# Optimization experiments

Hardware: AMD Instinct MI355X
Metric: run time of the kernel (lower is better)

## Reference

```python
import jax, jax.numpy as jnp
import numpy as np

IN_F, OUT_F, TASK_D, RANK, HID = 1024, 1024, 256, 8, 64
ALPHA = 8.0
SCALING = ALPHA / RANK  # 1.0


def setup_inputs() -> dict:
    key = jax.random.key(0)
    ks = jax.random.split(key, 12)
    s = 0.02
    return {
        "x": jax.random.normal(ks[0], (4, 2048, IN_F), dtype=jnp.float32),
        "base_out": jax.random.normal(ks[1], (4, 2048, OUT_F), dtype=jnp.float32),
        "task_emb": jax.random.normal(ks[2], (4, TASK_D), dtype=jnp.float32),
        # gen_a MLP: Linear(task_dim->hid) + GELU + Linear(hid->out*r)
        "Wa1": jax.random.normal(ks[3], (HID, TASK_D), dtype=jnp.float32) * s,
        "ba1": jnp.zeros((HID,), dtype=jnp.float32),
        "Wa2": jax.random.normal(ks[4], (OUT_F * RANK, HID), dtype=jnp.float32) * s,
        "ba2": jnp.zeros((OUT_F * RANK,), dtype=jnp.float32),
        # gen_b MLP: Linear(task_dim->hid) + GELU + Linear(hid->r*in)
        "Wb1": jax.random.normal(ks[5], (HID, TASK_D), dtype=jnp.float32) * s,
        "bb1": jnp.zeros((HID,), dtype=jnp.float32),
        "Wb2": jax.random.normal(ks[6], (RANK * IN_F, HID), dtype=jnp.float32) * s,
        "bb2": jnp.zeros((RANK * IN_F,), dtype=jnp.float32),
    }


def reference(x, base_out, task_emb, Wa1, ba1, Wa2, ba2, Wb1, bb1, Wb2, bb2):
    lead = x.shape[:-1]
    x2d = x.reshape(-1, IN_F)                      # (b_eff, in)
    b_eff = x2d.shape[0]
    # broadcast task_emb to b_eff rows (repeat + trim, as in torch)
    B = task_emb.shape[0]
    reps = (b_eff + B - 1) // B
    task_eff = jnp.tile(task_emb, (reps, 1))[:b_eff]  # (b_eff, task_dim)

    gelu = lambda t: jax.nn.gelu(t, approximate=False)
    h_a = gelu(task_eff @ Wa1.T + ba1)
    vec_a = h_a @ Wa2.T + ba2                      # (b_eff, out*r)
    h_b = gelu(task_eff @ Wb1.T + bb1)
    vec_b = h_b @ Wb2.T + bb2                      # (b_eff, r*in)

    a = vec_a.reshape(b_eff, OUT_F, RANK)
    b = vec_b.reshape(b_eff, RANK, IN_F)

    # dropout p=0 (eval): x passes through
    tmp = jnp.einsum('bi,bri->br', x2d, b)         # (b_eff, r)
    y_delta = jnp.einsum('br,bor->bo', tmp, a)     # (b_eff, out)
    y = base_out.reshape(-1, OUT_F) + SCALING * y_delta
    return y.reshape(*lead, OUT_F)
```

## Files before the change

kernel.cpp:

```cpp
#include <hip/hip_runtime.h>
#include <math.h>

#define IN_F   1024
#define OUT_F  1024
#define TASK_D 256
#define RANK   8
#define HID    64

__device__ __forceinline__ float gelu_exact(float v) {
    return 0.5f * v * (1.0f + erff(v * 0.70710678118654752f));
}

__global__ __launch_bounds__(256) void gen_kernel(
    const float* __restrict__ task_emb,
    const float* __restrict__ Wa1, const float* __restrict__ ba1,
    const float* __restrict__ Wa2, const float* __restrict__ ba2,
    const float* __restrict__ Wb1, const float* __restrict__ bb1,
    const float* __restrict__ Wb2, const float* __restrict__ bb2,
    float* __restrict__ vec_a_t, float* __restrict__ vec_b)
{
    const int gen = blockIdx.x >> 7;
    const int blk = blockIdx.x & 127;
    const float* __restrict__ W1 = gen ? Wb1 : Wa1;
    const float* __restrict__ b1 = gen ? bb1 : ba1;
    const float* __restrict__ W2 = gen ? Wb2 : Wa2;
    const float* __restrict__ b2 = gen ? bb2 : ba2;

    __shared__ float hs[4][HID];
    {
        const int j = threadIdx.x >> 2;
        const int t = threadIdx.x & 3;
        const float4* te = (const float4*)(task_emb + t * TASK_D);
        const float4* w  = (const float4*)(W1 + j * TASK_D);
        float acc = 0.f;
        #pragma unroll
        for (int d = 0; d < TASK_D / 4; ++d) {
            float4 a = te[d], b = w[d];
            acc += a.x * b.x + a.y * b.y + a.z * b.z + a.w * b.w;
        }
        hs[t][j] = gelu_exact(acc + b1[j]);
    }
    __syncthreads();

    const int lrow = threadIdx.x >> 2;
    const int q    = threadIdx.x & 3;
    const int o    = blk * 64 + lrow;

    const float4* w2 = (const float4*)(W2 + (size_t)o * HID + q * 16);
    float acc0 = 0.f, acc1 = 0.f, acc2 = 0.f, acc3 = 0.f;
    #pragma unroll
    for (int k = 0; k < 4; ++k) {
        float4 w = w2[k];
        const int kb = q * 16 + k * 4;
        acc0 += hs[0][kb] * w.x + hs[0][kb+1] * w.y + hs[0][kb+2] * w.z + hs[0][kb+3] * w.w;
        acc1 += hs[1][kb] * w.x + hs[1][kb+1] * w.y + hs[1][kb+2] * w.z + hs[1][kb+3] * w.w;
        acc2 += hs[2][kb] * w.x + hs[2][kb+1] * w.y + hs[2][kb+2] * w.z + hs[2][kb+3] * w.w;
        acc3 += hs[3][kb] * w.x + hs[3][kb+1] * w.y + hs[3][kb+2] * w.z + hs[3][kb+3] * w.w;
    }
    #pragma unroll
    for (int off = 1; off <= 2; off <<= 1) {
        acc0 += __shfl_xor(acc0, off, 64);
        acc1 += __shfl_xor(acc1, off, 64);
        acc2 += __shfl_xor(acc2, off, 64);
        acc3 += __shfl_xor(acc3, off, 64);
    }
    if (q == 0) {
        const float bb = b2[o];
        float v[4] = { acc0 + bb, acc1 + bb, acc2 + bb, acc3 + bb };
        if (gen == 0) {
            const int oo = o >> 3, r = o & 7;
            #pragma unroll
            for (int t = 0; t < 4; ++t)
                vec_a_t[t * (RANK * OUT_F) + r * OUT_F + oo] = v[t];
        } else {
            #pragma unroll
            for (int t = 0; t < 4; ++t)
                vec_b[t * (RANK * IN_F) + o] = v[t];
        }
    }
}

__global__ __launch_bounds__(256, 8) void apply_kernel(
    const float* __restrict__ x, const float* __restrict__ base_out,
    const float* __restrict__ vec_a_t, const float* __restrict__ vec_b,
    float* __restrict__ out, int g_per_task)
{
    const int t    = blockIdx.x / g_per_task;
    const int g    = blockIdx.x % g_per_task;
    const int wave = threadIdx.x >> 6;
    const int ln   = threadIdx.x & 63;

    const int j   = g * 4 + wave;
    const int row = t + 4 * j;

    const float* __restrict__ xr = x + (size_t)row * IN_F;
    const float* __restrict__ bt = vec_b + (size_t)t * (RANK * IN_F);

    float4 xv[4];
    #pragma unroll
    for (int c = 0; c < 4; ++c)
        xv[c] = *(const float4*)(xr + c * 256 + ln * 4);

    float acc[RANK];
    #pragma unroll
    for (int r = 0; r < RANK; ++r) acc[r] = 0.f;

    #pragma unroll
    for (int c = 0; c < 4; ++c) {
        const int k = c * 256 + ln * 4;
        #pragma unroll
        for (int r = 0; r < RANK; ++r) {
            const float4 bv = *(const float4*)(bt + r * IN_F + k);
            acc[r] += xv[c].x * bv.x + xv[c].y * bv.y + xv[c].z * bv.z + xv[c].w * bv.w;
        }
    }

    #pragma unroll
    for (int off = 1; off <= 32; off <<= 1) {
        #pragma unroll
        for (int r = 0; r < RANK; ++r)
            acc[r] += __shfl_xor(acc[r], off, 64);
    }

    const float* __restrict__ at = vec_a_t + (size_t)t * (RANK * OUT_F);
    const float* __restrict__ br = base_out + (size_t)row * OUT_F;
    float* __restrict__ orow = out + (size_t)row * OUT_F;

    float4 bo[4];
    #pragma unroll
    for (int c = 0; c < 4; ++c)
        bo[c] = *(const float4*)(br + c * 256 + ln * 4);

    #pragma unroll
    for (int c = 0; c < 4; ++c) {
        const int o = c * 256 + ln * 4;
        float4 rv = bo[c];
        #pragma unroll
        for (int r = 0; r < RANK; ++r) {
            const float4 af = *(const float4*)(at + r * OUT_F + o);
            rv.x += acc[r] * af.x;
            rv.y += acc[r] * af.y;
            rv.z += acc[r] * af.z;
            rv.w += acc[r] * af.w;
        }
        *(float4*)(orow + o) = rv;
    }
}

extern "C" void kernel_launch(void* const* d_in, const int* in_sizes, int n_in,
                              void* d_out, int out_size, void* d_ws, size_t ws_size,
                              hipStream_t stream) {
    const float* x        = (const float*)d_in[0];
    const float* base_out = (const float*)d_in[1];
    const float* task_emb = (const float*)d_in[2];
    const float* Wa1      = (const float*)d_in[3];
    const float* ba1      = (const float*)d_in[4];
    const float* Wa2      = (const float*)d_in[5];
    const float* ba2      = (const float*)d_in[6];
    const float* Wb1      = (const float*)d_in[7];
    const float* bb1      = (const float*)d_in[8];
    const float* Wb2      = (const float*)d_in[9];
    const float* bb2      = (const float*)d_in[10];
    float* out = (float*)d_out;

    float* vec_a_t = (float*)d_ws;
    float* vec_b   = vec_a_t + 4 * RANK * OUT_F;

    const int b_eff = in_sizes[0] / IN_F;

    gen_kernel<<<256, 256, 0, stream>>>(task_emb, Wa1, ba1, Wa2, ba2,
                                        Wb1, bb1, Wb2, bb2, vec_a_t, vec_b);

    const int nblk = b_eff / 4;
    apply_kernel<<<nblk, 256, 0, stream>>>(x, base_out, vec_a_t, vec_b, out,
                                           nblk / 4);
}
```

Before: 156.6 us.

## Process four rows per wave with per-task B and A factors held in registers

Each wave now handles four rows of the same task instead of one. It loads the task's vec_b slice (8x1024) into registers once, reuses it for all four rows' rank projections, then reloads registers with the vec_a slice and reuses that for all four output rows. The aim is to cut repeated L2/global reads of the generated LoRA factors by four. The cost is a large register footprint (128 floats per lane for the tile), occupancy lowered to 2 blocks per CU, and a grid four times smaller.

Result: faster. 143.6 us (-8.3%).

```diff
diff --git a/kernel.cpp b/kernel.cpp
--- a/kernel.cpp
+++ b/kernel.cpp
@@ -80,70 +80,100 @@
     }
 }
 
-__global__ __launch_bounds__(256, 8) void apply_kernel(
+__global__ __launch_bounds__(256, 2) void apply_kernel(
     const float* __restrict__ x, const float* __restrict__ base_out,
     const float* __restrict__ vec_a_t, const float* __restrict__ vec_b,
-    float* __restrict__ out, int g_per_task)
+    float* __restrict__ out, int waves_per_task)
 {
-    const int t    = blockIdx.x / g_per_task;
-    const int g    = blockIdx.x % g_per_task;
     const int wave = threadIdx.x >> 6;
     const int ln   = threadIdx.x & 63;
-
-    const int j   = g * 4 + wave;
-    const int row = t + 4 * j;
-
-    const float* __restrict__ xr = x + (size_t)row * IN_F;
+    const int gw   = blockIdx.x * 4 + wave;
+    const int t    = gw / waves_per_task;
+    const int u    = gw % waves_per_task;
+
     const float* __restrict__ bt = vec_b + (size_t)t * (RANK * IN_F);
-
-    float4 xv[4];
-    #pragma unroll
-    for (int c = 0; c < 4; ++c)
-        xv[c] = *(const float4*)(xr + c * 256 + ln * 4);
-
-    float acc[RANK];
-    #pragma unroll
-    for (int r = 0; r < RANK; ++r) acc[r] = 0.f;
-
-    #pragma unroll
-    for (int c = 0; c < 4; ++c) {
-        const int k = c * 256 + ln * 4;
-        #pragma unroll
-        for (int r = 0; r < RANK; ++r) {
-            const float4 bv = *(const float4*)(bt + r * IN_F + k);
-            acc[r] += xv[c].x * bv.x + xv[c].y * bv.y + xv[c].z * bv.z + xv[c].w * bv.w;
-        }
-    }
-
-    #pragma unroll
-    for (int off = 1; off <= 32; off <<= 1) {
-        #pragma unroll
-        for (int r = 0; r < RANK; ++r)
-            acc[r] += __shfl_xor(acc[r], off, 64);
+    float4 tb[RANK][4];
+    #pragma unroll
+    for (int r = 0; r < RANK; ++r)
+        #pragma unroll
+        for (int c = 0; c < 4; ++c)
+            tb[r][c] = *(const float4*)(bt + r * IN_F + c * 256 + ln * 4);
+
+    float tmp[4][RANK];
+
+    #pragma unroll
+    for (int ii = 0; ii < 2; ++ii) {
+        float4 xv[2][4];
+        #pragma unroll
+        for (int i = 0; i < 2; ++i) {
+            const int row = t + 4 * (u * 4 + ii * 2 + i);
+            const float* __restrict__ xr = x + (size_t)row * IN_F;
+            #pragma unroll
+            for (int c = 0; c < 4; ++c)
+                xv[i][c] = *(const float4*)(xr + c * 256 + ln * 4);
+        }
+        #pragma unroll
+        for (int i = 0; i < 2; ++i) {
+            float acc[RANK];
+            #pragma unroll
+            for (int r = 0; r < RANK; ++r) acc[r] = 0.f;
+            #pragma unroll
+            for (int c = 0; c < 4; ++c) {
+                #pragma unroll
+                for (int r = 0; r < RANK; ++r) {
+                    const float4 bv = tb[r][c];
+                    acc[r] += xv[i][c].x * bv.x + xv[i][c].y * bv.y
+                            + xv[i][c].z * bv.z + xv[i][c].w * bv.w;
+                }
+            }
+            #pragma unroll
+            for (int off = 1; off <= 32; off <<= 1) {
+                #pragma unroll
+                for (int r = 0; r < RANK; ++r)
+                    acc[r] += __shfl_xor(acc[r], off, 64);
+            }
+            #pragma unroll
+            for (int r = 0; r < RANK; ++r) tmp[ii * 2 + i][r] = acc[r];
+        }
     }
 
     const float* __restrict__ at = vec_a_t + (size_t)t * (RANK * OUT_F);
-    const float* __restrict__ br = base_out + (size_t)row * OUT_F;
-    float* __restrict__ orow = out + (size_t)row * OUT_F;
-
-    float4 bo[4];
-    #pragma unroll
-    for (int c = 0; c < 4; ++c)
-        bo[c] = *(const float4*)(br + c * 256 + ln * 4);
-
-    #pragma unroll
-    for (int c = 0; c < 4; ++c) {
-        const int o = c * 256 + ln * 4;
-        float4 rv = bo[c];
-        #pragma unroll
-        for (int r = 0; r < RANK; ++r) {
-            const float4 af = *(const float4*)(at + r * OUT_F + o);
-            rv.x += acc[r] * af.x;
-            rv.y += acc[r] * af.y;
-            rv.z += acc[r] * af.z;
-            rv.w += acc[r] * af.w;
-        }
-        *(float4*)(orow + o) = rv;
+    #pragma unroll
+    for (int r = 0; r < RANK; ++r)
+        #pragma unroll
+        for (int c = 0; c < 4; ++c)
+            tb[r][c] = *(const float4*)(at + r * OUT_F + c * 256 + ln * 4);
+
+    #pragma unroll
+    for (int ii = 0; ii < 2; ++ii) {
+        float4 bo[2][4];
+        #pragma unroll
+        for (int i = 0; i < 2; ++i) {
+            const int row = t + 4 * (u * 4 + ii * 2 + i);
+            const float* __restrict__ br = base_out + (size_t)row * OUT_F;
+            #pragma unroll
+            for (int c = 0; c < 4; ++c)
+                bo[i][c] = *(const float4*)(br + c * 256 + ln * 4);
+        }
+        #pragma unroll
+        for (int i = 0; i < 2; ++i) {
+            const int row = t + 4 * (u * 4 + ii * 2 + i);
+            float* __restrict__ orow = out + (size_t)row * OUT_F;
+            #pragma unroll
+            for (int c = 0; c < 4; ++c) {
+                float4 rv = bo[i][c];
+                #pragma unroll
+                for (int r = 0; r < RANK; ++r) {
+                    const float4 af = tb[r][c];
+                    const float s = tmp[ii * 2 + i][r];
+                    rv.x += s * af.x;
+                    rv.y += s * af.y;
+                    rv.z += s * af.z;
+                    rv.w += s * af.w;
+                }
+                *(float4*)(orow + c * 256 + ln * 4) = rv;
+            }
+        }
     }
 }
 
@@ -171,7 +201,7 @@
     gen_kernel<<<256, 256, 0, stream>>>(task_emb, Wa1, ba1, Wa2, ba2,
                                         Wb1, bb1, Wb2, bb2, vec_a_t, vec_b);
 
-    const int nblk = b_eff / 4;
+    const int nblk = b_eff / 16;
     apply_kernel<<<nblk, 256, 0, stream>>>(x, base_out, vec_a_t, vec_b, out,
-                                           nblk / 4);
-}
+                                           nblk);
+}
```

## Split apply kernel into separate x·B projection and output update kernels

Applied to the files above, without the earlier changes.

Splits the fused apply kernel into two kernels. tmp_kernel computes the rank-8 projection of each x row and writes it to a workspace buffer. out_kernel loads the vec_a tile once per thread into registers and reuses it across four rows to add the low-rank update to base_out. The aim is to cut repeated reloads of vec_a and raise memory-level parallelism. The cost is an extra launch and a small intermediate write and read.

New measurement: 149.5 us. 1.05x faster.

```diff
diff --git a/kernel.cpp b/kernel.cpp
--- a/kernel.cpp
+++ b/kernel.cpp
@@ -80,18 +80,16 @@
     }
 }
 
-__global__ __launch_bounds__(256, 8) void apply_kernel(
-    const float* __restrict__ x, const float* __restrict__ base_out,
-    const float* __restrict__ vec_a_t, const float* __restrict__ vec_b,
-    float* __restrict__ out, int g_per_task)
+__global__ __launch_bounds__(256) void tmp_kernel(
+    const float* __restrict__ x, const float* __restrict__ vec_b,
+    float* __restrict__ tmp, int waves_per_task)
 {
-    const int t    = blockIdx.x / g_per_task;
-    const int g    = blockIdx.x % g_per_task;
     const int wave = threadIdx.x >> 6;
     const int ln   = threadIdx.x & 63;
-
-    const int j   = g * 4 + wave;
-    const int row = t + 4 * j;
+    const int gw   = blockIdx.x * 4 + wave;
+    const int t    = gw / waves_per_task;
+    const int j    = gw % waves_per_task;
+    const int row  = t + 4 * j;
 
     const float* __restrict__ xr = x + (size_t)row * IN_F;
     const float* __restrict__ bt = vec_b + (size_t)t * (RANK * IN_F);
@@ -122,28 +120,52 @@
             acc[r] += __shfl_xor(acc[r], off, 64);
     }
 
+    if (ln == 0) {
+        float* __restrict__ tr = tmp + (size_t)row * RANK;
+        *(float4*)(tr)     = make_float4(acc[0], acc[1], acc[2], acc[3]);
+        *(float4*)(tr + 4) = make_float4(acc[4], acc[5], acc[6], acc[7]);
+    }
+}
+
+__global__ __launch_bounds__(256, 4) void out_kernel(
+    const float* __restrict__ base_out, const float* __restrict__ vec_a_t,
+    const float* __restrict__ tmp, float* __restrict__ out,
+    int blocks_per_task)
+{
+    const int t = blockIdx.x / blocks_per_task;
+    const int g = blockIdx.x % blocks_per_task;
+    const int o = threadIdx.x * 4;
+
     const float* __restrict__ at = vec_a_t + (size_t)t * (RANK * OUT_F);
-    const float* __restrict__ br = base_out + (size_t)row * OUT_F;
-    float* __restrict__ orow = out + (size_t)row * OUT_F;
-
-    float4 bo[4];
-    #pragma unroll
-    for (int c = 0; c < 4; ++c)
-        bo[c] = *(const float4*)(br + c * 256 + ln * 4);
-
-    #pragma unroll
-    for (int c = 0; c < 4; ++c) {
-        const int o = c * 256 + ln * 4;
-        float4 rv = bo[c];
+    float4 af[RANK];
+    #pragma unroll
+    for (int r = 0; r < RANK; ++r)
+        af[r] = *(const float4*)(at + r * OUT_F + o);
+
+    int   row[4];
+    float4 bo[4], t0[4], t1[4];
+    #pragma unroll
+    for (int i = 0; i < 4; ++i) {
+        row[i] = t + 4 * (g * 4 + i);
+        bo[i] = *(const float4*)(base_out + (size_t)row[i] * OUT_F + o);
+        const float* __restrict__ tr = tmp + (size_t)row[i] * RANK;
+        t0[i] = *(const float4*)(tr);
+        t1[i] = *(const float4*)(tr + 4);
+    }
+
+    #pragma unroll
+    for (int i = 0; i < 4; ++i) {
+        const float s[RANK] = { t0[i].x, t0[i].y, t0[i].z, t0[i].w,
+                                t1[i].x, t1[i].y, t1[i].z, t1[i].w };
+        float4 rv = bo[i];
         #pragma unroll
         for (int r = 0; r < RANK; ++r) {
-            const float4 af = *(const float4*)(at + r * OUT_F + o);
-            rv.x += acc[r] * af.x;
-            rv.y += acc[r] * af.y;
-            rv.z += acc[r] * af.z;
-            rv.w += acc[r] * af.w;
-        }
-        *(float4*)(orow + o) = rv;
+            rv.x += s[r] * af[r].x;
+            rv.y += s[r] * af[r].y;
+            rv.z += s[r] * af[r].z;
+            rv.w += s[r] * af[r].w;
+        }
+        *(float4*)(out + (size_t)row[i] * OUT_F + o) = rv;
     }
 }
 
@@ -165,13 +187,17 @@
 
     float* vec_a_t = (float*)d_ws;
     float* vec_b   = vec_a_t + 4 * RANK * OUT_F;
+    float* tmp     = vec_b   + 4 * RANK * IN_F;
 
     const int b_eff = in_sizes[0] / IN_F;
 
     gen_kernel<<<256, 256, 0, stream>>>(task_emb, Wa1, ba1, Wa2, ba2,
                                         Wb1, bb1, Wb2, bb2, vec_a_t, vec_b);
 
-    const int nblk = b_eff / 4;
-    apply_kernel<<<nblk, 256, 0, stream>>>(x, base_out, vec_a_t, vec_b, out,
-                                           nblk / 4);
-}
+    const int nblk2 = b_eff / 4;
+    tmp_kernel<<<nblk2, 256, 0, stream>>>(x, vec_b, tmp, b_eff / 4);
+
+    const int nblk3 = b_eff / 4;
+    out_kernel<<<nblk3, 256, 0, stream>>>(base_out, vec_a_t, tmp, out,
+                                          nblk3 / 4);
+}
```

## Share LoRA A factors across rows via LDS and widen generator grid

Applied to the files above, without the earlier changes.

In the apply kernel, each wave still computes the rank-8 projection for its own row, but the results now go through shared memory. The output phase then has each thread load its slice of the A factors once and reuse it across the block's four rows, instead of reloading A per row. The generator kernel now uses 512 blocks of 32 output rows each, with an 8-lane reduction, to spread the weight-matrix reads over more blocks. This adds a block-wide barrier and lowers the occupancy hint from 8 to 6 blocks per CU.

New measurement: 151.3 us. 1.03x faster.

```diff
diff --git a/kernel.cpp b/kernel.cpp
--- a/kernel.cpp
+++ b/kernel.cpp
@@ -19,8 +19,8 @@
     const float* __restrict__ Wb2, const float* __restrict__ bb2,
     float* __restrict__ vec_a_t, float* __restrict__ vec_b)
 {
-    const int gen = blockIdx.x >> 7;
-    const int blk = blockIdx.x & 127;
+    const int gen = blockIdx.x >> 8;
+    const int blk = blockIdx.x & 255;
     const float* __restrict__ W1 = gen ? Wb1 : Wa1;
     const float* __restrict__ b1 = gen ? bb1 : ba1;
     const float* __restrict__ W2 = gen ? Wb2 : Wa2;
@@ -42,23 +42,23 @@
     }
     __syncthreads();
 
-    const int lrow = threadIdx.x >> 2;
-    const int q    = threadIdx.x & 3;
-    const int o    = blk * 64 + lrow;
+    const int lrow = threadIdx.x >> 3;
+    const int q    = threadIdx.x & 7;
+    const int o    = blk * 32 + lrow;
 
-    const float4* w2 = (const float4*)(W2 + (size_t)o * HID + q * 16);
+    const float4* w2 = (const float4*)(W2 + (size_t)o * HID + q * 8);
     float acc0 = 0.f, acc1 = 0.f, acc2 = 0.f, acc3 = 0.f;
     #pragma unroll
-    for (int k = 0; k < 4; ++k) {
+    for (int k = 0; k < 2; ++k) {
         float4 w = w2[k];
-        const int kb = q * 16 + k * 4;
+        const int kb = q * 8 + k * 4;
         acc0 += hs[0][kb] * w.x + hs[0][kb+1] * w.y + hs[0][kb+2] * w.z + hs[0][kb+3] * w.w;
         acc1 += hs[1][kb] * w.x + hs[1][kb+1] * w.y + hs[1][kb+2] * w.z + hs[1][kb+3] * w.w;
         acc2 += hs[2][kb] * w.x + hs[2][kb+1] * w.y + hs[2][kb+2] * w.z + hs[2][kb+3] * w.w;
         acc3 += hs[3][kb] * w.x + hs[3][kb+1] * w.y + hs[3][kb+2] * w.z + hs[3][kb+3] * w.w;
     }
     #pragma unroll
-    for (int off = 1; off <= 2; off <<= 1) {
+    for (int off = 1; off <= 4; off <<= 1) {
         acc0 += __shfl_xor(acc0, off, 64);
         acc1 += __shfl_xor(acc1, off, 64);
         acc2 += __shfl_xor(acc2, off, 64);
@@ -80,70 +80,86 @@
     }
 }
 
-__global__ __launch_bounds__(256, 8) void apply_kernel(
+__global__ __launch_bounds__(256, 6) void apply_kernel(
     const float* __restrict__ x, const float* __restrict__ base_out,
     const float* __restrict__ vec_a_t, const float* __restrict__ vec_b,
-    float* __restrict__ out, int g_per_task)
+    float* __restrict__ out, int blocks_per_task)
 {
-    const int t    = blockIdx.x / g_per_task;
-    const int g    = blockIdx.x % g_per_task;
+    const int t    = blockIdx.x / blocks_per_task;
+    const int g    = blockIdx.x % blocks_per_task;
     const int wave = threadIdx.x >> 6;
     const int ln   = threadIdx.x & 63;
 
-    const int j   = g * 4 + wave;
-    const int row = t + 4 * j;
+    __shared__ float tmps[4][RANK];
 
-    const float* __restrict__ xr = x + (size_t)row * IN_F;
-    const float* __restrict__ bt = vec_b + (size_t)t * (RANK * IN_F);
+    {
+        const int row = t + 4 * (g * 4 + wave);
+        const float* __restrict__ xr = x + (size_t)row * IN_F;
+        const float* __restrict__ bt = vec_b + (size_t)t * (RANK * IN_F);
 
-    float4 xv[4];
+        float4 xv[4];
+        #pragma unroll
+        for (int c = 0; c < 4; ++c)
+            xv[c] = *(const float4*)(xr + c * 256 + ln * 4);
+
+        float acc[RANK];
+        #pragma unroll
+        for (int r = 0; r < RANK; ++r) acc[r] = 0.f;
+
+        #pragma unroll
+        for (int c = 0; c < 4; ++c) {
+            const int k = c * 256 + ln * 4;
+            #pragma unroll
+            for (int r = 0; r < RANK; ++r) {
+                const float4 bv = *(const float4*)(bt + r * IN_F + k);
+                acc[r] += xv[c].x * bv.x + xv[c].y * bv.y
+                        + xv[c].z * bv.z + xv[c].w * bv.w;
+            }
+        }
+
+        #pragma unroll
+        for (int off = 1; off <= 32; off <<= 1) {
+            #pragma unroll
+            for (int r = 0; r < RANK; ++r)
+                acc[r] += __shfl_xor(acc[r], off, 64);
+        }
+
+        if (ln == 0) {
+            #pragma unroll
+            for (int r = 0; r < RANK; ++r)
+                tmps[wave][r] = acc[r];
+        }
+    }
+    __syncthreads();
+
+    const int o = threadIdx.x * 4;
+    const float* __restrict__ at = vec_a_t + (size_t)t * (RANK * OUT_F);
+
+    float4 af[RANK];
     #pragma unroll
-    for (int c = 0; c < 4; ++c)
-        xv[c] = *(const float4*)(xr + c * 256 + ln * 4);
+    for (int r = 0; r < RANK; ++r)
+        af[r] = *(const float4*)(at + r * OUT_F + o);
 
-    float acc[RANK];
+    float4 bo[4];
     #pragma unroll
-    for (int r = 0; r < RANK; ++r) acc[r] = 0.f;
-
-    #pragma unroll
-    for (int c = 0; c < 4; ++c) {
-        const int k = c * 256 + ln * 4;
-        #pragma unroll
-        for (int r = 0; r < RANK; ++r) {
-            const float4 bv = *(const float4*)(bt + r * IN_F + k);
-            acc[r] += xv[c].x * bv.x + xv[c].y * bv.y + xv[c].z * bv.z + xv[c].w * bv.w;
-        }
+    for (int i = 0; i < 4; ++i) {
+        const int row = t + 4 * (g * 4 + i);
+        bo[i] = *(const float4*)(base_out + (size_t)row * OUT_F + o);
     }
 
     #pragma unroll
-    for (int off = 1; off <= 32; off <<= 1) {
-        #pragma unroll
-        for (int r = 0; r < RANK; ++r)
-            acc[r] += __shfl_xor(acc[r], off, 64);
-    }
-
-    const float* __restrict__ at = vec_a_t + (size_t)t * (RANK * OUT_F);
-    const float* __restrict__ br = base_out + (size_t)row * OUT_F;
-    float* __restrict__ orow = out + (size_t)row * OUT_F;
-
-    float4 bo[4];
-    #pragma unroll
-    for (int c = 0; c < 4; ++c)
-        bo[c] = *(const float4*)(br + c * 256 + ln * 4);
-
-    #pragma unroll
-    for (int c = 0; c < 4; ++c) {
-        const int o = c * 256 + ln * 4;
-        float4 rv = bo[c];
+    for (int i = 0; i < 4; ++i) {
+        const int row = t + 4 * (g * 4 + i);
+        float4 rv = bo[i];
         #pragma unroll
         for (int r = 0; r < RANK; ++r) {
-            const float4 af = *(const float4*)(at + r * OUT_F + o);
-            rv.x += acc[r] * af.x;
-            rv.y += acc[r] * af.y;
-            rv.z += acc[r] * af.z;
-            rv.w += acc[r] * af.w;
+            const float s = tmps[i][r];
+            rv.x += s * af[r].x;
+            rv.y += s * af[r].y;
+            rv.z += s * af[r].z;
+            rv.w += s * af[r].w;
         }
-        *(float4*)(orow + o) = rv;
+        *(float4*)(out + (size_t)row * OUT_F + o) = rv;
     }
 }
 
@@ -168,7 +184,7 @@
 
     const int b_eff = in_sizes[0] / IN_F;
 
-    gen_kernel<<<256, 256, 0, stream>>>(task_emb, Wa1, ba1, Wa2, ba2,
+    gen_kernel<<<512, 256, 0, stream>>>(task_emb, Wa1, ba1, Wa2, ba2,
                                         Wb1, bb1, Wb2, bb2, vec_a_t, vec_b);
 
     const int nblk = b_eff / 4;
```
